# Kernel tuning notes

Measured on AMD Instinct MI355X. Metric: run time of the kernel, lower is better.

Reference implementation:

```python
import jax, jax.numpy as jnp
import numpy as np

TEMP = 1.75   # temp_schedule(epoch=5, warmup=10): 2.5 - 1.5*0.5
ALPHA = 0.5   # blend_schedule(epoch=5): 0.2 + 0.6*0.5
EPS = 1e-5
HEADS = 2


def _ln(x, g, b):
    mu = x.mean(-1, keepdims=True)
    var = ((x - mu) ** 2).mean(-1, keepdims=True)
    return (x - mu) * jax.lax.rsqrt(var + EPS) * g + b


def _gelu(x):
    return jax.nn.gelu(x, approximate=False)  # torch nn.GELU default = exact erf


def _attn_pool(x, ln_g, ln_b, in_w, in_b, out_w, out_b):
    # x: [N, T, E]; nn.MultiheadAttention self-attention then mean over T
    N, T, E = x.shape
    Dh = E // HEADS
    xn = _ln(x, ln_g, ln_b)
    qkv = xn @ in_w + in_b                      # [N, T, 3E] (in_w stored [E, 3E])
    q, k, v = jnp.split(qkv, 3, axis=-1)
    q = q.reshape(N, T, HEADS, Dh).transpose(0, 2, 1, 3)
    k = k.reshape(N, T, HEADS, Dh).transpose(0, 2, 1, 3)
    v = v.reshape(N, T, HEADS, Dh).transpose(0, 2, 1, 3)
    scores = jnp.einsum('nhqd,nhkd->nhqk', q, k) / jnp.sqrt(jnp.float32(Dh))
    a = jax.nn.softmax(scores, axis=-1)
    o = jnp.einsum('nhqk,nhkd->nhqd', a, v).transpose(0, 2, 1, 3).reshape(N, T, E)
    o = o @ out_w + out_b                       # [N, T, E]
    return o.mean(axis=1)                       # [N, E]


def setup_inputs() -> dict:
    key = jax.random.key(0)
    ks = iter(jax.random.split(key, 40))
    B, L, T, D = 4, 24, 400, 1024
    H = D // 2  # 512
    G = 4       # groups
    s = 0.02
    r = lambda shp: jax.random.normal(next(ks), shp, dtype=jnp.float32) * s
    inp = {
        'x': jax.random.normal(next(ks), (B, L, T, D), dtype=jnp.float32),
        'mlp_alpha': jnp.ones((L,), jnp.float32),
        # shared MLP: LN -> Linear(D,H) -> GELU -> Linear(H,H)
        's_ln_g': jnp.ones((D,), jnp.float32), 's_ln_b': jnp.zeros((D,), jnp.float32),
        's_w1': r((D, H)), 's_b1': jnp.zeros((H,), jnp.float32),
        's_w2': r((H, H)), 's_b2': jnp.zeros((H,), jnp.float32),
        # 4 group MLPs (stacked)
        'g_ln_g': jnp.ones((G, D), jnp.float32), 'g_ln_b': jnp.zeros((G, D), jnp.float32),
        'g_w1': r((G, D, H)), 'g_b1': jnp.zeros((G, H), jnp.float32),
        'g_w2': r((G, H, H)), 'g_b2': jnp.zeros((G, H), jnp.float32),
        # TimeAttentionPool (shared module): LN + MHA(512, 2 heads) + out_proj
        'p_ln_g': jnp.ones((H,), jnp.float32), 'p_ln_b': jnp.zeros((H,), jnp.float32),
        'p_in_w': r((H, 3 * H)), 'p_in_b': jnp.zeros((3 * H,), jnp.float32),
        'p_out_w': r((H, H)), 'p_out_b': jnp.zeros((H,), jnp.float32),
        # router: Linear(512,128) -> GELU -> Linear(128,1) -> sigmoid(/temp)
        'r_w1': r((H, 128)), 'r_b1': jnp.zeros((128,), jnp.float32),
        'r_w2': r((128, 1)), 'r_b2': jnp.zeros((1,), jnp.float32),
        # post norms
        'pn_g': jnp.ones((H,), jnp.float32), 'pn_b': jnp.zeros((H,), jnp.float32),
        'pnf_g': jnp.ones((H,), jnp.float32), 'pnf_b': jnp.zeros((H,), jnp.float32),
        # classifier 512 -> 256 -> 128 -> 2
        'c_w1': r((H, H // 2)), 'c_b1': jnp.zeros((H // 2,), jnp.float32),
        'c_w2': r((H // 2, H // 4)), 'c_b2': jnp.zeros((H // 4,), jnp.float32),
        'c_w3': r((H // 4, 2)), 'c_b3': jnp.zeros((2,), jnp.float32),
    }
    return inp


def reference(x, mlp_alpha, s_ln_g, s_ln_b, s_w1, s_b1, s_w2, s_b2,
              g_ln_g, g_ln_b, g_w1, g_b1, g_w2, g_b2,
              p_ln_g, p_ln_b, p_in_w, p_in_b, p_out_w, p_out_b,
              r_w1, r_b1, r_w2, r_b2, pn_g, pn_b, pnf_g, pnf_b,
              c_w1, c_b1, c_w2, c_b2, c_w3, c_b3):
    B, L, T, D = x.shape
    G = g_w1.shape[0]
    S = L // G  # group_size = 6; expert i uses group i // S
    H = s_w1.shape[1]

    # shared MLP over all experts at once (dropout inactive in eval)
    xs = _ln(x, s_ln_g, s_ln_b)                              # [B,L,T,D]
    shared = _gelu(xs @ s_w1 + s_b1) @ s_w2 + s_b2           # [B,L,T,H]

    # group MLPs: experts i//S -> group; reshape L -> (G, S)
    xg = x.reshape(B, G, S, T, D)
    xgn = _ln(xg, g_ln_g[:, None, None, :], g_ln_b[:, None, None, :])
    hg = _gelu(jnp.einsum('bgstd,gdh->bgsth', xgn, g_w1) + g_b1[None, :, None, None, :])
    grp = jnp.einsum('bgsth,ghk->bgstk', hg, g_w2) + g_b2[None, :, None, None, :]
    grp = grp.reshape(B, L, T, H)

    weighted = shared + mlp_alpha[None, :, None, None] * grp  # [B,L,T,H]

    # attn-pool every expert stream (fold L into batch)
    time_pooled = _attn_pool(weighted.reshape(B * L, T, H),
                             p_ln_g, p_ln_b, p_in_w, p_in_b, p_out_w, p_out_b)
    time_pooled = time_pooled.reshape(B, L, H)               # [B,L,H]

    # router
    rh = _gelu(time_pooled @ r_w1 + r_b1)
    logits_r = (rh @ r_w2 + r_b2)[..., 0]                    # [B,L]
    learned = jax.nn.sigmoid(logits_r / TEMP)
    routing_weights = ALPHA * learned + (1.0 - ALPHA) / L

    # soft fusion over experts
    fusion = (weighted * routing_weights[:, :, None, None]).sum(axis=1)  # [B,T,H]
    fusion = _ln(fusion, pn_g, pn_b).mean(axis=1)            # [B,H]

    shared_mean = shared.mean(axis=1)                        # [B,T,H]
    time_ctx = _attn_pool(shared_mean, p_ln_g, p_ln_b, p_in_w, p_in_b, p_out_w, p_out_b)

    fused_all = _ln(fusion, pnf_g, pnf_b) + _ln(time_ctx, pnf_g, pnf_b)  # [B,H]

    h = _gelu(fused_all @ c_w1 + c_b1)
    h = _gelu(h @ c_w2 + c_b2)
    logits = h @ c_w3 + c_b3                                 # [B,2]
    return logits, routing_weights, fused_all, time_pooled
```

## Files before the change

kernel.cpp:

```cpp
#include <hip/hip_runtime.h>
#include <stdint.h>


typedef float f32x4 __attribute__((ext_vector_type(4)));
typedef short bf16x8 __attribute__((ext_vector_type(8)));

__device__ __forceinline__ float bf2f(unsigned short u) {
  return __uint_as_float(((unsigned int)u) << 16);
}
__device__ __forceinline__ unsigned short f2bf(float f) {
  unsigned int u = __float_as_uint(f);
  u += 0x7fffu + ((u >> 16) & 1u);
  return (unsigned short)(u >> 16);
}
__device__ __forceinline__ float gelu_f(float x) {
  return 0.5f * x * (1.0f + erff(x * 0.70710678118654752440f));
}

template <int EPI, int GROUPED>
__global__ __launch_bounds__(256) void gemm_bt(
    const unsigned short* __restrict__ A, const unsigned short* __restrict__ WT,
    const float* __restrict__ bias, unsigned short* __restrict__ Cout,
    const unsigned short* __restrict__ addbuf, const float* __restrict__ alpha_vec,
    unsigned short* __restrict__ vtbuf, int K, int N, int ldout, int Mslice) {
  const int tid = (int)threadIdx.x;
  const int w = tid >> 6, lane = tid & 63, g = lane >> 4, ql = lane & 15;
  const int bm = blockIdx.x, bn = blockIdx.y, z = blockIdx.z;
  const int wr = w >> 1, wc = w & 1;
  const int n0 = bn * 128;

  int rowbase, rows_here;
  const unsigned short* wt = WT;
  const float* bs = bias;
  float alpha = 0.f;
  if (GROUPED) {
    const int l_idx = z % 24;
    const int grp = l_idx / 6;
    rowbase = z * Mslice + bm * 128;
    rows_here = Mslice - bm * 128;
    if (rows_here > 128) rows_here = 128;
    wt = WT + (size_t)grp * (size_t)N * (size_t)K;
    bs = bias + (size_t)grp * (size_t)N;
    if (EPI == 2) alpha = alpha_vec[l_idx];
  } else {
    rowbase = bm * 128;
    rows_here = Mslice - bm * 128;
    if (rows_here > 128) rows_here = 128;
  }

  __shared__ __align__(16) unsigned short sA[128 * 56];
  __shared__ __align__(16) unsigned short sB[128 * 56];

  f32x4 acc[4][4];
#pragma unroll
  for (int i = 0; i < 4; ++i)
#pragma unroll
    for (int j = 0; j < 4; ++j) acc[i][j] = (f32x4){0.f, 0.f, 0.f, 0.f};

  const int q0c = tid, q1c = tid + 256;
  const int r0 = q0c >> 2, s0 = q0c & 3;
  const int r1 = q1c >> 2, s1 = q1c & 3;
  const int r0c = r0 < rows_here ? r0 : rows_here - 1;
  const int r1c = r1 < rows_here ? r1 : rows_here - 1;
  const unsigned short* a0p = A + (size_t)(rowbase + r0c) * K + s0 * 8;
  const unsigned short* a1p = A + (size_t)(rowbase + r1c) * K + s1 * 8;
  const unsigned short* b0p = wt + (size_t)(n0 + r0) * K + s0 * 8;
  const unsigned short* b1p = wt + (size_t)(n0 + r1) * K + s1 * 8;

  const int nsteps = K >> 5;
  bf16x8 ra0 = *(const bf16x8*)a0p, ra1 = *(const bf16x8*)a1p;
  bf16x8 rb0 = *(const bf16x8*)b0p, rb1 = *(const bf16x8*)b1p;

  for (int s = 0; s < nsteps; ++s) {
    __syncthreads();
    *(bf16x8*)(sA + r0 * 56 + s0 * 8) = ra0;
    *(bf16x8*)(sA + r1 * 56 + s1 * 8) = ra1;
    *(bf16x8*)(sB + r0 * 56 + s0 * 8) = rb0;
    *(bf16x8*)(sB + r1 * 56 + s1 * 8) = rb1;
    __syncthreads();
    if (s + 1 < nsteps) {
      const int k0 = (s + 1) << 5;
      ra0 = *(const bf16x8*)(a0p + k0);
      ra1 = *(const bf16x8*)(a1p + k0);
      rb0 = *(const bf16x8*)(b0p + k0);
      rb1 = *(const bf16x8*)(b1p + k0);
    }
    bf16x8 af[4], bfr[4];
#pragma unroll
    for (int mi = 0; mi < 4; ++mi)
      af[mi] = *(const bf16x8*)(sA + (wr * 64 + mi * 16 + ql) * 56 + g * 8);
#pragma unroll
    for (int ni = 0; ni < 4; ++ni)
      bfr[ni] = *(const bf16x8*)(sB + (wc * 64 + ni * 16 + ql) * 56 + g * 8);
#pragma unroll
    for (int mi = 0; mi < 4; ++mi)
#pragma unroll
      for (int ni = 0; ni < 4; ++ni)
        acc[mi][ni] =
            __builtin_amdgcn_mfma_f32_16x16x32_bf16(af[mi], bfr[ni], acc[mi][ni], 0, 0, 0);
  }

#pragma unroll
  for (int mi = 0; mi < 4; ++mi) {
#pragma unroll
    for (int ni = 0; ni < 4; ++ni) {
      const int col = n0 + wc * 64 + ni * 16 + ql;
      const float bb = bs[col];
#pragma unroll
      for (int r = 0; r < 4; ++r) {
        const int rloc = wr * 64 + mi * 16 + 4 * g + r;
        if (rloc >= rows_here) continue;
        const int grow = rowbase + rloc;
        float v = acc[mi][ni][r] + bb;
        if (EPI == 1) v = gelu_f(v);
        if (EPI == 0 || EPI == 1) {
          Cout[(size_t)grow * ldout + col] = f2bf(v);
        } else if (EPI == 2) {
          const float sh = bf2f(addbuf[(size_t)grow * ldout + col]);
          Cout[(size_t)grow * ldout + col] = f2bf(sh + alpha * v);
        } else {
          if (col < 1024) {
            Cout[(size_t)grow * ldout + col] = f2bf(v);
          } else {
            vtbuf[(size_t)grow * 512 + (col - 1024)] = f2bf(v);
          }
        }
      }
    }
  }
}

__global__ void transpose_v(const unsigned short* __restrict__ vbuf,
                            unsigned short* __restrict__ vt) {
  const int p = blockIdx.z;
  const int h = p & 1, nst = p >> 1;
  const int t0 = blockIdx.x * 32, d0 = blockIdx.y * 32;
  __shared__ unsigned short tile[32][33];
  const int tx = threadIdx.x, ty = threadIdx.y;
#pragma unroll
  for (int i = 0; i < 4; ++i) {
    const int t = t0 + ty + i * 8;
    if (t < 400)
      tile[ty + i * 8][tx] = vbuf[((size_t)nst * 400 + t) * 512 + h * 256 + d0 + tx];
  }
  __syncthreads();
  const int t = t0 + tx;
  if (t < 400) {
#pragma unroll
    for (int i = 0; i < 4; ++i)
      vt[((size_t)p * 256 + d0 + ty + i * 8) * 400 + t] = tile[tx][ty + i * 8];
  }
}

__global__ __launch_bounds__(256, 2) void attn_fwd(const unsigned short* __restrict__ qk,
                                                   const unsigned short* __restrict__ vt,
                                                   unsigned short* __restrict__ outb) {
  const int nb = (int)gridDim.x;
  int flat = (int)blockIdx.x;
  flat = (flat & 7) * (nb >> 3) + (flat >> 3);
  const int qt = flat % 7;
  const int h = (flat / 7) & 1;
  const int n = flat / 14;
  const int q0 = qt * 64;

  const int tid = (int)threadIdx.x;
  const int w = tid >> 6, lane = tid & 63, g = lane >> 4, ql = lane & 15;

  __shared__ __align__(16) unsigned short slab[400 * 32];
  __shared__ __align__(16) unsigned short Pc[4][512];
  __shared__ float rs[4][16];

  const int qr = q0 + w * 16 + ql;
  const int qrc = qr < 400 ? qr : 399;
  const unsigned short* qp = qk + ((size_t)n * 400 + qrc) * 1024 + h * 256 + g * 8;
  bf16x8 qf[8];
#pragma unroll
  for (int d0 = 0; d0 < 8; ++d0) qf[d0] = *(const bf16x8*)(qp + d0 * 32);

  f32x4 st[25];
#pragma unroll
  for (int kf = 0; kf < 25; ++kf) st[kf] = (f32x4){0.f, 0.f, 0.f, 0.f};

  const unsigned short* kbase = qk + (size_t)n * 400 * 1024 + 512 + h * 256;
  for (int d0 = 0; d0 < 8; ++d0) {
    bf16x8 stg[7];
#pragma unroll
    for (int c = 0; c < 7; ++c) {
      const int q = tid + c * 256;
      const int r = q >> 2, slot = q & 3;
      if (r < 400)
        stg[c] = *(const bf16x8*)(kbase + (size_t)r * 1024 + d0 * 32 + slot * 8);
    }
    __syncthreads();
#pragma unroll
    for (int c = 0; c < 7; ++c) {
      const int q = tid + c * 256;
      const int r = q >> 2, slot = q & 3;
      if (r < 400) *(bf16x8*)(slab + r * 32 + (slot ^ ((r >> 1) & 3)) * 8) = stg[c];
    }
    __syncthreads();
#pragma unroll
    for (int kf = 0; kf < 25; ++kf) {
      const int r = kf * 16 + ql;
      bf16x8 kfr = *(const bf16x8*)(slab + r * 32 + ((g ^ ((r >> 1) & 3)) * 8));
      st[kf] = __builtin_amdgcn_mfma_f32_16x16x32_bf16(kfr, qf[d0], st[kf], 0, 0, 0);
    }
  }

  const float sc = 0.0625f;
  float m = -3.0e38f;
#pragma unroll
  for (int kf = 0; kf < 25; ++kf)
    m = fmaxf(m, fmaxf(fmaxf(st[kf][0], st[kf][1]), fmaxf(st[kf][2], st[kf][3])));
  m = fmaxf(m, __shfl_xor(m, 16));
  m = fmaxf(m, __shfl_xor(m, 32));
  float sum = 0.f;
  uint2 pp[25];
#pragma unroll
  for (int kf = 0; kf < 25; ++kf) {
    float e0 = expf((st[kf][0] - m) * sc);
    float e1 = expf((st[kf][1] - m) * sc);
    float e2 = expf((st[kf][2] - m) * sc);
    float e3 = expf((st[kf][3] - m) * sc);
    sum += (e0 + e1) + (e2 + e3);
    pp[kf].x = (unsigned int)f2bf(e0) | ((unsigned int)f2bf(e1) << 16);
    pp[kf].y = (unsigned int)f2bf(e2) | ((unsigned int)f2bf(e3) << 16);
  }
  sum += __shfl_xor(sum, 16);
  sum += __shfl_xor(sum, 32);
  if (g == 0) rs[w][ql] = sum;

  f32x4 oacc[16];
#pragma unroll
  for (int nf = 0; nf < 16; ++nf) oacc[nf] = (f32x4){0.f, 0.f, 0.f, 0.f};

  unsigned short* Pw = Pc[w];
  const unsigned short* vbase = vt + (size_t)(n * 2 + h) * 256 * 400;
  for (int kt = 0; kt < 13; ++kt) {
    const int k0 = kt * 32;
    bf16x8 stg[4];
#pragma unroll
    for (int c = 0; c < 4; ++c) {
      const int q = tid + c * 256;
      const int r = q >> 2, slot = q & 3;
      int kc = k0 + slot * 8;
      if (kc >= 400) kc = 0;
      stg[c] = *(const bf16x8*)(vbase + (size_t)r * 400 + kc);
    }
    __syncthreads();
#pragma unroll
    for (int c = 0; c < 4; ++c) {
      const int q = tid + c * 256;
      const int r = q >> 2, slot = q & 3;
      *(bf16x8*)(slab + r * 32 + (slot ^ ((r >> 1) & 3)) * 8) = stg[c];
    }
    {
      const int kf0 = 2 * kt;
      *(uint2*)(Pw + ql * 32 + 4 * g) = pp[kf0];
      uint2 hi = (kf0 + 1 < 25) ? pp[kf0 + 1] : (uint2){0u, 0u};
      *(uint2*)(Pw + ql * 32 + 16 + 4 * g) = hi;
    }
    __syncthreads();
    bf16x8 pa = *(const bf16x8*)(Pw + ql * 32 + g * 8);
#pragma unroll
    for (int nf = 0; nf < 16; ++nf) {
      const int r = nf * 16 + ql;
      bf16x8 vb = *(const bf16x8*)(slab + r * 32 + ((g ^ ((r >> 1) & 3)) * 8));
      oacc[nf] = __builtin_amdgcn_mfma_f32_16x16x32_bf16(pa, vb, oacc[nf], 0, 0, 0);
    }
  }

  const float inv0 = 1.f / rs[w][4 * g + 0];
  const float inv1 = 1.f / rs[w][4 * g + 1];
  const float inv2 = 1.f / rs[w][4 * g + 2];
  const float inv3 = 1.f / rs[w][4 * g + 3];
#pragma unroll
  for (int nf = 0; nf < 16; ++nf) {
#pragma unroll
    for (int r = 0; r < 4; ++r) {
      const int qrow = q0 + w * 16 + 4 * g + r;
      if (qrow < 400) {
        const float invr = (r == 0) ? inv0 : (r == 1) ? inv1 : (r == 2) ? inv2 : inv3;
        outb[((size_t)n * 400 + qrow) * 512 + h * 256 + nf * 16 + ql] =
            f2bf(oacc[nf][r] * invr);
      }
    }
  }
}

template <int TIN, int TOUT>
__global__ void ln_rows(const void* __restrict__ inv, void* __restrict__ outv,
                        const float* __restrict__ gam, const float* __restrict__ bet,
                        int C) {
  const int row = blockIdx.x, t = (int)threadIdx.x;
  float x0, x1, x2, x3;
  if (TIN == 0) {
    float4 v = ((const float4*)inv)[(size_t)row * (C >> 2) + t];
    x0 = v.x; x1 = v.y; x2 = v.z; x3 = v.w;
  } else {
    ushort4 v = ((const ushort4*)inv)[(size_t)row * (C >> 2) + t];
    x0 = bf2f(v.x); x1 = bf2f(v.y); x2 = bf2f(v.z); x3 = bf2f(v.w);
  }
  float s1 = x0 + x1 + x2 + x3;
  float s2 = x0 * x0 + x1 * x1 + x2 * x2 + x3 * x3;
  for (int mlane = 1; mlane < 64; mlane <<= 1) {
    s1 += __shfl_xor(s1, mlane);
    s2 += __shfl_xor(s2, mlane);
  }
  __shared__ float red[8];
  const int nw = blockDim.x >> 6;
  if ((t & 63) == 0) {
    red[t >> 6] = s1;
    red[4 + (t >> 6)] = s2;
  }
  __syncthreads();
  s1 = 0.f; s2 = 0.f;
  for (int i = 0; i < nw; ++i) {
    s1 += red[i];
    s2 += red[4 + i];
  }
  const float mu = s1 / C;
  const float var = s2 / C - mu * mu;
  const float rstd = rsqrtf(var + 1e-5f);
  float y0 = (x0 - mu) * rstd, y1 = (x1 - mu) * rstd, y2 = (x2 - mu) * rstd,
        y3 = (x3 - mu) * rstd;
  if (gam) {
    const int c = t * 4;
    y0 = y0 * gam[c + 0] + bet[c + 0];
    y1 = y1 * gam[c + 1] + bet[c + 1];
    y2 = y2 * gam[c + 2] + bet[c + 2];
    y3 = y3 * gam[c + 3] + bet[c + 3];
  }
  if (TOUT == 0) {
    ushort4 o;
    o.x = f2bf(y0); o.y = f2bf(y1); o.z = f2bf(y2); o.w = f2bf(y3);
    ((ushort4*)outv)[(size_t)row * (C >> 2) + t] = o;
  } else {
    float4 o;
    o.x = y0; o.y = y1; o.z = y2; o.w = y3;
    ((float4*)outv)[(size_t)row * (C >> 2) + t] = o;
  }
}

__global__ void transpose_w(const float* __restrict__ W, const float* __restrict__ scale,
                            unsigned short* __restrict__ WT, int K, int N) {
  __shared__ float tile[32][33];
  const int k0 = blockIdx.x * 32, n0 = blockIdx.y * 32, zg = blockIdx.z;
  const float* Wz = W + (size_t)zg * K * N;
  const float* sz = scale ? scale + (size_t)zg * K : (const float*)0;
  unsigned short* WTz = WT + (size_t)zg * (size_t)K * N;
  const int tx = threadIdx.x, ty = threadIdx.y;
#pragma unroll
  for (int i = 0; i < 4; ++i)
    tile[ty + i * 8][tx] = Wz[(size_t)(k0 + ty + i * 8) * N + n0 + tx];
  __syncthreads();
#pragma unroll
  for (int i = 0; i < 4; ++i) {
    const int nn = n0 + ty + i * 8;
    const int kk = k0 + tx;
    float v = tile[tx][ty + i * 8];
    if (sz) v *= sz[kk];
    WTz[(size_t)nn * K + kk] = f2bf(v);
  }
}

__global__ void transpose_wf(const float* __restrict__ W, float* __restrict__ WT, int K,
                             int N) {
  __shared__ float tile[32][33];
  const int k0 = blockIdx.x * 32, n0 = blockIdx.y * 32;
  const int tx = threadIdx.x, ty = threadIdx.y;
#pragma unroll
  for (int i = 0; i < 4; ++i) {
    const int k = k0 + ty + i * 8;
    if (k < K && n0 + tx < N) tile[ty + i * 8][tx] = W[(size_t)k * N + n0 + tx];
  }
  __syncthreads();
#pragma unroll
  for (int i = 0; i < 4; ++i) {
    const int nn = n0 + ty + i * 8;
    const int kk = k0 + tx;
    if (nn < N && kk < K) WT[(size_t)nn * K + kk] = tile[tx][ty + i * 8];
  }
}

#define BF_KC 16
__global__ void bias_fold_part(const float* __restrict__ W, const float* __restrict__ lb,
                               float* __restrict__ part, int K, int N) {
  const int zg = blockIdx.z;
  const int n = blockIdx.x * 256 + (int)threadIdx.x;
  const int kc = blockIdx.y;
  const int kpc = K / BF_KC;
  const float* Wz = W + (size_t)zg * K * N;
  const float* lbz = lb + (size_t)zg * K;
  float acc = 0.f;
  const int k1 = (kc + 1) * kpc;
  for (int k = kc * kpc; k < k1; ++k) acc += lbz[k] * Wz[(size_t)k * N + n];
  part[((size_t)zg * BF_KC + kc) * N + n] = acc;
}
__global__ void bias_fold_final(const float* __restrict__ part, const float* __restrict__ b,
                                float* __restrict__ beff, int N) {
  const int zg = blockIdx.y;
  const int n = blockIdx.x * 256 + (int)threadIdx.x;
  float acc = b[(size_t)zg * N + n];
#pragma unroll
  for (int c = 0; c < BF_KC; ++c) acc += part[((size_t)zg * BF_KC + c) * N + n];
  beff[(size_t)zg * N + n] = acc;
}

__global__ void mean_l(const unsigned short* __restrict__ sh, float* __restrict__ out) {
  const int i = blockIdx.x * 256 + (int)threadIdx.x;
  if (i >= 4 * 400 * 512) return;
  const int b = i / (400 * 512);
  const int rem = i - b * (400 * 512);
  float acc = 0.f;
  for (int l = 0; l < 24; ++l) acc += bf2f(sh[(size_t)(b * 24 + l) * 204800 + rem]);
  out[i] = acc * (1.f / 24.f);
}

__global__ void mean_t_bf16(const unsigned short* __restrict__ in, float* __restrict__ out,
                            int Ns) {
  const int i = blockIdx.x * 256 + (int)threadIdx.x;
  if (i >= Ns * 512) return;
  const int nstr = i >> 9, c = i & 511;
  float acc = 0.f;
  for (int t = 0; t < 400; ++t) acc += bf2f(in[((size_t)nstr * 400 + t) * 512 + c]);
  out[i] = acc * (1.f / 400.f);
}

__global__ void mean_t_f32(const float* __restrict__ in, float* __restrict__ out, int Ns) {
  const int i = blockIdx.x * 256 + (int)threadIdx.x;
  if (i >= Ns * 512) return;
  const int nstr = i >> 9, c = i & 511;
  float acc = 0.f;
  for (int t = 0; t < 400; ++t) acc += in[((size_t)nstr * 400 + t) * 512 + c];
  out[i] = acc * (1.f / 400.f);
}

__global__ void fuse_k(const unsigned short* __restrict__ wgt, const float* __restrict__ rw,
                       float* __restrict__ out) {
  const int i = blockIdx.x * 256 + (int)threadIdx.x;
  if (i >= 4 * 400 * 512) return;
  const int b = i / (400 * 512);
  const int rem = i - b * (400 * 512);
  float acc = 0.f;
  for (int l = 0; l < 24; ++l)
    acc += rw[b * 24 + l] * bf2f(wgt[(size_t)(b * 24 + l) * 204800 + rem]);
  out[i] = acc;
}

template <int WLAYOUT>
__global__ void gemv_wave(const float* __restrict__ A, const float* __restrict__ Wm,
                          const float* __restrict__ b, float* __restrict__ C, int M, int K,
                          int N, int act) {
  const int wid = (int)(blockIdx.x * (blockDim.x >> 6)) + ((int)threadIdx.x >> 6);
  const int lane = (int)threadIdx.x & 63;
  if (wid >= M * N) return;
  const int row = wid / N, col = wid - row * N;
  const float* a = A + (size_t)row * K;
  float acc = 0.f;
  if (WLAYOUT) {
    const float* wt = Wm + (size_t)col * K;
    for (int k = lane; k < K; k += 64) acc += a[k] * wt[k];
  } else {
    for (int k = lane; k < K; k += 64) acc += a[k] * Wm[(size_t)k * N + col];
  }
#pragma unroll
  for (int d = 1; d < 64; d <<= 1) acc += __shfl_xor(acc, d);
  if (lane == 0) {
    acc += b[col];
    if (act) acc = gelu_f(acc);
    C[wid] = acc;
  }
}

__global__ void routing_k(const float* __restrict__ lr, float* __restrict__ o1,
                          float* __restrict__ o2) {
  const int i = (int)threadIdx.x;
  if (i < 96) {
    const float v = 0.5f / (1.f + expf(-lr[i] * (1.f / 1.75f))) + (0.5f / 24.f);
    o1[i] = v;
    o2[i] = v;
  }
}

__global__ void add_k(const float* __restrict__ a, const float* __restrict__ b,
                      float* __restrict__ o1, float* __restrict__ o2, int n) {
  const int i = blockIdx.x * 256 + (int)threadIdx.x;
  if (i < n) {
    const float v = a[i] + b[i];
    o1[i] = v;
    o2[i] = v;
  }
}

extern "C" void kernel_launch(void* const* d_in, const int* in_sizes, int n_in,
                              void* d_out, int out_size, void* d_ws, size_t ws_size,
                              hipStream_t stream) {
  const float* x = (const float*)d_in[0];
  const float* mlp_alpha = (const float*)d_in[1];
  const float* s_ln_g = (const float*)d_in[2];
  const float* s_ln_b = (const float*)d_in[3];
  const float* s_w1 = (const float*)d_in[4];
  const float* s_b1 = (const float*)d_in[5];
  const float* s_w2 = (const float*)d_in[6];
  const float* s_b2 = (const float*)d_in[7];
  const float* g_ln_g = (const float*)d_in[8];
  const float* g_ln_b = (const float*)d_in[9];
  const float* g_w1 = (const float*)d_in[10];
  const float* g_b1 = (const float*)d_in[11];
  const float* g_w2 = (const float*)d_in[12];
  const float* g_b2 = (const float*)d_in[13];
  const float* p_ln_g = (const float*)d_in[14];
  const float* p_ln_b = (const float*)d_in[15];
  const float* p_in_w = (const float*)d_in[16];
  const float* p_in_b = (const float*)d_in[17];
  const float* p_out_w = (const float*)d_in[18];
  const float* p_out_b = (const float*)d_in[19];
  const float* r_w1 = (const float*)d_in[20];
  const float* r_b1 = (const float*)d_in[21];
  const float* r_w2 = (const float*)d_in[22];
  const float* r_b2 = (const float*)d_in[23];
  const float* pn_g = (const float*)d_in[24];
  const float* pn_b = (const float*)d_in[25];
  const float* pnf_g = (const float*)d_in[26];
  const float* pnf_b = (const float*)d_in[27];
  const float* c_w1 = (const float*)d_in[28];
  const float* c_b1 = (const float*)d_in[29];
  const float* c_w2 = (const float*)d_in[30];
  const float* c_b2 = (const float*)d_in[31];
  const float* c_w3 = (const float*)d_in[32];
  const float* c_b3 = (const float*)d_in[33];

  float* out = (float*)d_out;
  uint8_t* ws = (uint8_t*)d_ws;

  size_t off = 0;
  auto alloc = [&](size_t bytes) -> size_t {
    size_t o = off;
    off += (bytes + 255) & ~(size_t)255;
    return o;
  };
  const size_t off_xhat = alloc(38400ull * 1024 * 2);
  const size_t off_h = alloc(38400ull * 512 * 2);
  const size_t off_shared = alloc(38400ull * 512 * 2);
  const size_t off_weighted = alloc(38400ull * 512 * 2);
  const size_t off_qk = alloc(38400ull * 1024 * 2);
  const size_t off_pooled = alloc(96ull * 512 * 4);
  const size_t off_rh = alloc(96ull * 128 * 4);
  const size_t off_lr = alloc(96ull * 4);
  const size_t off_rw = alloc(96ull * 4);
  const size_t off_smean = alloc(4ull * 400 * 512 * 4);
  const size_t off_wn2 = alloc(1600ull * 512 * 2);
  const size_t off_qk2 = alloc(1600ull * 1024 * 2);
  const size_t off_vbuf2 = alloc(1600ull * 512 * 2);
  const size_t off_vt2 = alloc(4ull * 2 * 256 * 400 * 2);
  const size_t off_ao2 = alloc(1600ull * 512 * 2);
  const size_t off_pooled2 = alloc(4ull * 512 * 4);
  const size_t off_tctx = alloc(4ull * 512 * 4);
  const size_t off_fusion = alloc(4ull * 400 * 512 * 4);
  const size_t off_fln = alloc(4ull * 400 * 512 * 4);
  const size_t off_fvec = alloc(4ull * 512 * 4);
  const size_t off_fa = alloc(4ull * 512 * 4);
  const size_t off_fb = alloc(4ull * 512 * 4);
  const size_t off_fall = alloc(4ull * 512 * 4);
  const size_t off_c1 = alloc(4ull * 256 * 4);
  const size_t off_c2 = alloc(4ull * 128 * 4);
  const size_t off_sw1T = alloc(512ull * 1024 * 2);
  const size_t off_sw2T = alloc(512ull * 512 * 2);
  const size_t off_gw1T = alloc(4ull * 512 * 1024 * 2);
  const size_t off_gw2T = alloc(4ull * 512 * 512 * 2);
  const size_t off_pinT = alloc(1536ull * 512 * 2);
  const size_t off_sb1e = alloc(512ull * 4);
  const size_t off_gb1e = alloc(4ull * 512 * 4);
  const size_t off_pinbe = alloc(1536ull * 4);
  const size_t off_bfp_s = alloc((size_t)BF_KC * 512 * 4);
  const size_t off_bfp_g = alloc(4ull * BF_KC * 512 * 4);
  const size_t off_bfp_p = alloc((size_t)BF_KC * 1536 * 4);
  const size_t off_powT = alloc(512ull * 512 * 4);
  const size_t off_rw1T = alloc(128ull * 512 * 4);
  const size_t off_cw1T = alloc(256ull * 512 * 4);
  const size_t off_cw2T = alloc(128ull * 256 * 4);
  const size_t off_wn = off_xhat;
  const size_t off_vbuf = off_xhat + 38400ull * 512 * 2;
  const size_t off_vt = off_shared;
  const size_t off_ao = off_h;
  if (off > ws_size) return;

  unsigned short* xhat = (unsigned short*)(ws + off_xhat);
  unsigned short* hbuf = (unsigned short*)(ws + off_h);
  unsigned short* sharedb = (unsigned short*)(ws + off_shared);
  unsigned short* weighted = (unsigned short*)(ws + off_weighted);
  unsigned short* qk = (unsigned short*)(ws + off_qk);
  unsigned short* wn = (unsigned short*)(ws + off_wn);
  unsigned short* vbuf = (unsigned short*)(ws + off_vbuf);
  unsigned short* vt = (unsigned short*)(ws + off_vt);
  unsigned short* ao = (unsigned short*)(ws + off_ao);
  float* pooled = (float*)(ws + off_pooled);
  float* rh = (float*)(ws + off_rh);
  float* lr = (float*)(ws + off_lr);
  float* rw = (float*)(ws + off_rw);
  float* smean = (float*)(ws + off_smean);
  unsigned short* wn2 = (unsigned short*)(ws + off_wn2);
  unsigned short* qk2 = (unsigned short*)(ws + off_qk2);
  unsigned short* vbuf2 = (unsigned short*)(ws + off_vbuf2);
  unsigned short* vt2 = (unsigned short*)(ws + off_vt2);
  unsigned short* ao2 = (unsigned short*)(ws + off_ao2);
  float* pooled2 = (float*)(ws + off_pooled2);
  float* tctx = (float*)(ws + off_tctx);
  float* fusion = (float*)(ws + off_fusion);
  float* fln = (float*)(ws + off_fln);
  float* fvec = (float*)(ws + off_fvec);
  float* fa = (float*)(ws + off_fa);
  float* fb = (float*)(ws + off_fb);
  float* fall = (float*)(ws + off_fall);
  float* c1 = (float*)(ws + off_c1);
  float* c2 = (float*)(ws + off_c2);
  unsigned short* sw1T = (unsigned short*)(ws + off_sw1T);
  unsigned short* sw2T = (unsigned short*)(ws + off_sw2T);
  unsigned short* gw1T = (unsigned short*)(ws + off_gw1T);
  unsigned short* gw2T = (unsigned short*)(ws + off_gw2T);
  unsigned short* pinT = (unsigned short*)(ws + off_pinT);
  float* sb1e = (float*)(ws + off_sb1e);
  float* gb1e = (float*)(ws + off_gb1e);
  float* pinbe = (float*)(ws + off_pinbe);
  float* bfp_s = (float*)(ws + off_bfp_s);
  float* bfp_g = (float*)(ws + off_bfp_g);
  float* bfp_p = (float*)(ws + off_bfp_p);
  float* powT = (float*)(ws + off_powT);
  float* rw1T = (float*)(ws + off_rw1T);
  float* cw1T = (float*)(ws + off_cw1T);
  float* cw2T = (float*)(ws + off_cw2T);

  transpose_w<<<dim3(32, 16, 1), dim3(32, 8), 0, stream>>>(s_w1, s_ln_g, sw1T, 1024, 512);
  transpose_w<<<dim3(16, 16, 1), dim3(32, 8), 0, stream>>>(s_w2, (const float*)0, sw2T, 512, 512);
  transpose_w<<<dim3(32, 16, 4), dim3(32, 8), 0, stream>>>(g_w1, g_ln_g, gw1T, 1024, 512);
  transpose_w<<<dim3(16, 16, 4), dim3(32, 8), 0, stream>>>(g_w2, (const float*)0, gw2T, 512, 512);
  transpose_w<<<dim3(16, 48, 1), dim3(32, 8), 0, stream>>>(p_in_w, p_ln_g, pinT, 512, 1536);
  transpose_wf<<<dim3(16, 16), dim3(32, 8), 0, stream>>>(p_out_w, powT, 512, 512);
  transpose_wf<<<dim3(16, 4), dim3(32, 8), 0, stream>>>(r_w1, rw1T, 512, 128);
  transpose_wf<<<dim3(16, 8), dim3(32, 8), 0, stream>>>(c_w1, cw1T, 512, 256);
  transpose_wf<<<dim3(8, 4), dim3(32, 8), 0, stream>>>(c_w2, cw2T, 256, 128);
  bias_fold_part<<<dim3(2, BF_KC, 1), 256, 0, stream>>>(s_w1, s_ln_b, bfp_s, 1024, 512);
  bias_fold_final<<<dim3(2, 1), 256, 0, stream>>>(bfp_s, s_b1, sb1e, 512);
  bias_fold_part<<<dim3(2, BF_KC, 4), 256, 0, stream>>>(g_w1, g_ln_b, bfp_g, 1024, 512);
  bias_fold_final<<<dim3(2, 4), 256, 0, stream>>>(bfp_g, g_b1, gb1e, 512);
  bias_fold_part<<<dim3(6, BF_KC, 1), 256, 0, stream>>>(p_in_w, p_ln_b, bfp_p, 512, 1536);
  bias_fold_final<<<dim3(6, 1), 256, 0, stream>>>(bfp_p, p_in_b, pinbe, 1536);

  ln_rows<0, 0><<<38400, 256, 0, stream>>>(x, xhat, (const float*)0, (const float*)0, 1024);

  gemm_bt<1, 0><<<dim3(300, 4, 1), 256, 0, stream>>>(xhat, sw1T, sb1e, hbuf,
      (const unsigned short*)0, (const float*)0, (unsigned short*)0, 1024, 512, 512, 38400);
  gemm_bt<0, 0><<<dim3(300, 4, 1), 256, 0, stream>>>(hbuf, sw2T, s_b2, sharedb,
      (const unsigned short*)0, (const float*)0, (unsigned short*)0, 512, 512, 512, 38400);
  mean_l<<<3200, 256, 0, stream>>>(sharedb, smean);

  gemm_bt<1, 1><<<dim3(4, 4, 96), 256, 0, stream>>>(xhat, gw1T, gb1e, hbuf,
      (const unsigned short*)0, (const float*)0, (unsigned short*)0, 1024, 512, 512, 400);
  gemm_bt<2, 1><<<dim3(4, 4, 96), 256, 0, stream>>>(hbuf, gw2T, g_b2, weighted,
      sharedb, mlp_alpha, (unsigned short*)0, 512, 512, 512, 400);

  ln_rows<1, 0><<<38400, 128, 0, stream>>>(weighted, wn, (const float*)0, (const float*)0, 512);
  gemm_bt<3, 0><<<dim3(300, 12, 1), 256, 0, stream>>>(wn, pinT, pinbe, qk,
      (const unsigned short*)0, (const float*)0, vbuf, 512, 1536, 1024, 38400);
  transpose_v<<<dim3(13, 8, 192), dim3(32, 8), 0, stream>>>(vbuf, vt);
  attn_fwd<<<dim3(14 * 96), 256, 0, stream>>>(qk, vt, ao);
  mean_t_bf16<<<192, 256, 0, stream>>>(ao, pooled, 96);
  gemv_wave<1><<<12288, 256, 0, stream>>>(pooled, powT, p_out_b, out + 2152, 96, 512, 512, 0);

  gemv_wave<1><<<3072, 256, 0, stream>>>(out + 2152, rw1T, r_b1, rh, 96, 512, 128, 1);
  gemv_wave<0><<<24, 256, 0, stream>>>(rh, r_w2, r_b2, lr, 96, 128, 1, 0);
  routing_k<<<1, 128, 0, stream>>>(lr, out + 8, rw);

  fuse_k<<<3200, 256, 0, stream>>>(weighted, rw, fusion);
  ln_rows<0, 1><<<1600, 128, 0, stream>>>(fusion, fln, pn_g, pn_b, 512);
  mean_t_f32<<<8, 256, 0, stream>>>(fln, fvec, 4);

  ln_rows<0, 0><<<1600, 128, 0, stream>>>(smean, wn2, (const float*)0, (const float*)0, 512);
  gemm_bt<3, 0><<<dim3(13, 12, 1), 256, 0, stream>>>(wn2, pinT, pinbe, qk2,
      (const unsigned short*)0, (const float*)0, vbuf2, 512, 1536, 1024, 1600);
  transpose_v<<<dim3(13, 8, 8), dim3(32, 8), 0, stream>>>(vbuf2, vt2);
  attn_fwd<<<dim3(14 * 4), 256, 0, stream>>>(qk2, vt2, ao2);
  mean_t_bf16<<<8, 256, 0, stream>>>(ao2, pooled2, 4);
  gemv_wave<1><<<512, 256, 0, stream>>>(pooled2, powT, p_out_b, tctx, 4, 512, 512, 0);

  ln_rows<0, 1><<<4, 128, 0, stream>>>(fvec, fa, pnf_g, pnf_b, 512);
  ln_rows<0, 1><<<4, 128, 0, stream>>>(tctx, fb, pnf_g, pnf_b, 512);
  add_k<<<8, 256, 0, stream>>>(fa, fb, out + 104, fall, 2048);

  gemv_wave<1><<<256, 256, 0, stream>>>(fall, cw1T, c_b1, c1, 4, 512, 256, 1);
  gemv_wave<1><<<128, 256, 0, stream>>>(c1, cw2T, c_b2, c2, 4, 256, 128, 1);
  gemv_wave<0><<<2, 256, 0, stream>>>(c2, c_w3, c_b3, out, 4, 128, 2, 0);
}
```

Baseline: 845.8 us.

## Remap GEMM blocks per XCD, widen LDS padding, vectorize mean_l and fuse_k

Non-grouped GEMM launches now remap the linear block index so that each of the 8 XCDs gets a contiguous range of tiles. This is meant to improve L2 reuse of the A rows and weight tiles. The LDS row stride grows from 56 to 72 elements to change the bank-conflict pattern, which raises shared memory per block. The mean_l and fuse_k reductions each process 4 elements per thread with ushort4 loads and float4 stores, launching a quarter as many blocks.

```diff
diff --git a/kernel.cpp b/kernel.cpp
--- a/kernel.cpp
+++ b/kernel.cpp
@@ -4,6 +4,8 @@
 
 typedef float f32x4 __attribute__((ext_vector_type(4)));
 typedef short bf16x8 __attribute__((ext_vector_type(8)));
+
+#define LP 72
 
 __device__ __forceinline__ float bf2f(unsigned short u) {
   return __uint_as_float(((unsigned int)u) << 16);
@@ -25,8 +27,24 @@
     unsigned short* __restrict__ vtbuf, int K, int N, int ldout, int Mslice) {
   const int tid = (int)threadIdx.x;
   const int w = tid >> 6, lane = tid & 63, g = lane >> 4, ql = lane & 15;
-  const int bm = blockIdx.x, bn = blockIdx.y, z = blockIdx.z;
+  const int z = blockIdx.z;
   const int wr = w >> 1, wc = w & 1;
+
+  int bm, bn;
+  if (!GROUPED) {
+    const int nbm = (int)gridDim.x, nbn = (int)gridDim.y;
+    const int nb = nbm * nbn;
+    const int lin = (int)blockIdx.x + nbm * (int)blockIdx.y;
+    const int q = nb >> 3, r8 = nb & 7;
+    const int xcd = lin & 7, c = lin >> 3;
+    const int base = (xcd < r8) ? xcd * (q + 1) : r8 * (q + 1) + (xcd - r8) * q;
+    const int widx = base + c;
+    bm = widx / nbn;
+    bn = widx - bm * nbn;
+  } else {
+    bm = (int)blockIdx.x;
+    bn = (int)blockIdx.y;
+  }
   const int n0 = bn * 128;
 
   int rowbase, rows_here;
@@ -48,8 +66,8 @@
     if (rows_here > 128) rows_here = 128;
   }
 
-  __shared__ __align__(16) unsigned short sA[128 * 56];
-  __shared__ __align__(16) unsigned short sB[128 * 56];
+  __shared__ __align__(16) unsigned short sA[128 * LP];
+  __shared__ __align__(16) unsigned short sB[128 * LP];
 
   f32x4 acc[4][4];
 #pragma unroll
@@ -73,10 +91,10 @@
 
   for (int s = 0; s < nsteps; ++s) {
     __syncthreads();
-    *(bf16x8*)(sA + r0 * 56 + s0 * 8) = ra0;
-    *(bf16x8*)(sA + r1 * 56 + s1 * 8) = ra1;
-    *(bf16x8*)(sB + r0 * 56 + s0 * 8) = rb0;
-    *(bf16x8*)(sB + r1 * 56 + s1 * 8) = rb1;
+    *(bf16x8*)(sA + r0 * LP + s0 * 8) = ra0;
+    *(bf16x8*)(sA + r1 * LP + s1 * 8) = ra1;
+    *(bf16x8*)(sB + r0 * LP + s0 * 8) = rb0;
+    *(bf16x8*)(sB + r1 * LP + s1 * 8) = rb1;
     __syncthreads();
     if (s + 1 < nsteps) {
       const int k0 = (s + 1) << 5;
@@ -88,10 +106,10 @@
     bf16x8 af[4], bfr[4];
 #pragma unroll
     for (int mi = 0; mi < 4; ++mi)
-      af[mi] = *(const bf16x8*)(sA + (wr * 64 + mi * 16 + ql) * 56 + g * 8);
+      af[mi] = *(const bf16x8*)(sA + (wr * 64 + mi * 16 + ql) * LP + g * 8);
 #pragma unroll
     for (int ni = 0; ni < 4; ++ni)
-      bfr[ni] = *(const bf16x8*)(sB + (wc * 64 + ni * 16 + ql) * 56 + g * 8);
+      bfr[ni] = *(const bf16x8*)(sB + (wc * 64 + ni * 16 + ql) * LP + g * 8);
 #pragma unroll
     for (int mi = 0; mi < 4; ++mi)
 #pragma unroll
@@ -409,12 +427,18 @@
 
 __global__ void mean_l(const unsigned short* __restrict__ sh, float* __restrict__ out) {
   const int i = blockIdx.x * 256 + (int)threadIdx.x;
-  if (i >= 4 * 400 * 512) return;
-  const int b = i / (400 * 512);
-  const int rem = i - b * (400 * 512);
-  float acc = 0.f;
-  for (int l = 0; l < 24; ++l) acc += bf2f(sh[(size_t)(b * 24 + l) * 204800 + rem]);
-  out[i] = acc * (1.f / 24.f);
+  if (i >= 4 * 400 * 512 / 4) return;
+  const int b = i / (400 * 512 / 4);
+  const int rem4 = i - b * (400 * 512 / 4);
+  float a0 = 0.f, a1 = 0.f, a2 = 0.f, a3 = 0.f;
+  for (int l = 0; l < 24; ++l) {
+    ushort4 v = *(const ushort4*)(sh + (size_t)(b * 24 + l) * 204800 + rem4 * 4);
+    a0 += bf2f(v.x); a1 += bf2f(v.y); a2 += bf2f(v.z); a3 += bf2f(v.w);
+  }
+  float4 o;
+  o.x = a0 * (1.f / 24.f); o.y = a1 * (1.f / 24.f);
+  o.z = a2 * (1.f / 24.f); o.w = a3 * (1.f / 24.f);
+  ((float4*)out)[i] = o;
 }
 
 __global__ void mean_t_bf16(const unsigned short* __restrict__ in, float* __restrict__ out,
@@ -439,13 +463,19 @@
 __global__ void fuse_k(const unsigned short* __restrict__ wgt, const float* __restrict__ rw,
                        float* __restrict__ out) {
   const int i = blockIdx.x * 256 + (int)threadIdx.x;
-  if (i >= 4 * 400 * 512) return;
-  const int b = i / (400 * 512);
-  const int rem = i - b * (400 * 512);
-  float acc = 0.f;
-  for (int l = 0; l < 24; ++l)
-    acc += rw[b * 24 + l] * bf2f(wgt[(size_t)(b * 24 + l) * 204800 + rem]);
-  out[i] = acc;
+  if (i >= 4 * 400 * 512 / 4) return;
+  const int b = i / (400 * 512 / 4);
+  const int rem4 = i - b * (400 * 512 / 4);
+  float a0 = 0.f, a1 = 0.f, a2 = 0.f, a3 = 0.f;
+  for (int l = 0; l < 24; ++l) {
+    const float wv = rw[b * 24 + l];
+    ushort4 v = *(const ushort4*)(wgt + (size_t)(b * 24 + l) * 204800 + rem4 * 4);
+    a0 += wv * bf2f(v.x); a1 += wv * bf2f(v.y);
+    a2 += wv * bf2f(v.z); a3 += wv * bf2f(v.w);
+  }
+  float4 o;
+  o.x = a0; o.y = a1; o.z = a2; o.w = a3;
+  ((float4*)out)[i] = o;
 }
 
 template <int WLAYOUT>
@@ -653,7 +683,7 @@
       (const unsigned short*)0, (const float*)0, (unsigned short*)0, 1024, 512, 512, 38400);
   gemm_bt<0, 0><<<dim3(300, 4, 1), 256, 0, stream>>>(hbuf, sw2T, s_b2, sharedb,
       (const unsigned short*)0, (const float*)0, (unsigned short*)0, 512, 512, 512, 38400);
-  mean_l<<<3200, 256, 0, stream>>>(sharedb, smean);
+  mean_l<<<800, 256, 0, stream>>>(sharedb, smean);
 
   gemm_bt<1, 1><<<dim3(4, 4, 96), 256, 0, stream>>>(xhat, gw1T, gb1e, hbuf,
       (const unsigned short*)0, (const float*)0, (unsigned short*)0, 1024, 512, 512, 400);
@@ -672,7 +702,7 @@
   gemv_wave<0><<<24, 256, 0, stream>>>(rh, r_w2, r_b2, lr, 96, 128, 1, 0);
   routing_k<<<1, 128, 0, stream>>>(lr, out + 8, rw);
 
-  fuse_k<<<3200, 256, 0, stream>>>(weighted, rw, fusion);
+  fuse_k<<<800, 256, 0, stream>>>(weighted, rw, fusion);
   ln_rows<0, 1><<<1600, 128, 0, stream>>>(fusion, fln, pn_g, pn_b, 512);
   mean_t_f32<<<8, 256, 0, stream>>>(fln, fvec, 4);
 
```

After: 823.2 us. 1.03x faster.
